# Kernel optimization log

Measured on AMD Instinct MI355X. Metric: run time of the kernel, lower is better.

Reference implementation:

```python
import jax, jax.numpy as jnp
import numpy as np

FT_IN = 40960
VFT_IN = 640


def _sparse_linear(indices, values, W, b, B):
    # y[r] = sum_{k: row[k]==r} values[k] * W[:, col[k]]  + b
    # W: [out, in]; gather columns as rows of W.T -> [nnz, out]
    rows = indices[0]
    cols = indices[1]
    contrib = W.T[cols] * values[:, None]          # [nnz, out]
    acc = jnp.zeros((B, W.shape[0]), dtype=W.dtype).at[rows].add(contrib)
    return acc + b


def setup_inputs() -> dict:
    B = 8192
    NNZ_PER_POS = 32
    NNZ = B * NNZ_PER_POS
    FT_OUT = 256
    key = jax.random.key(0)
    ks = jax.random.split(key, 8)

    def make_indices(k):
        kb, kf = jax.random.split(k)
        bids = jax.random.randint(kb, (NNZ,), 0, B, dtype=jnp.int32)
        fids = jax.random.randint(kf, (NNZ,), 0, FT_IN, dtype=jnp.int32)
        return jnp.stack([bids, fids], axis=0)  # [2, NNZ]

    s = 1.0 / np.sqrt(FT_IN)
    sv = 1.0 / np.sqrt(VFT_IN)
    so = 1.0 / np.sqrt(2 * FT_OUT)
    return {
        "stm_indices": make_indices(ks[0]),
        "nstm_indices": make_indices(ks[1]),
        "values": jnp.ones((NNZ,), dtype=jnp.float32),
        "size": B,
        "ft_w": jax.random.uniform(ks[2], (FT_OUT, FT_IN), jnp.float32, -s, s),
        "ft_b": jax.random.uniform(ks[3], (FT_OUT,), jnp.float32, -s, s),
        "fft_w": jax.random.uniform(ks[4], (FT_OUT, VFT_IN), jnp.float32, -sv, sv),
        "fft_b": jax.random.uniform(ks[5], (FT_OUT,), jnp.float32, -sv, sv),
        "out_w": jax.random.uniform(ks[6], (1, 2 * FT_OUT), jnp.float32, -so, so),
        "out_b": jax.random.uniform(ks[7], (1,), jnp.float32, -so, so),
    }


def reference(stm_indices, nstm_indices, values, size, ft_w, ft_b, fft_w, fft_b, out_w, out_b):
    B = size
    # factorized (virtual) feature indices: column % 640
    v_stm = jnp.stack([stm_indices[0], stm_indices[1] % VFT_IN], axis=0)
    v_nstm = jnp.stack([nstm_indices[0], nstm_indices[1] % VFT_IN], axis=0)

    stm_ft = _sparse_linear(stm_indices, values, ft_w, ft_b, B) + \
             _sparse_linear(v_stm, values, fft_w, fft_b, B) - fft_b  # bias added once in torch? no:
    # NOTE: torch adds both biases (ft.bias and fft.bias); undo the subtraction above.
    stm_ft = stm_ft + fft_b
    nstm_ft = _sparse_linear(nstm_indices, values, ft_w, ft_b, B) + \
              _sparse_linear(v_nstm, values, fft_w, fft_b, B)

    hidden = jnp.clip(jnp.concatenate([stm_ft, nstm_ft], axis=1), 0.0, 1.0)  # [B, 2*ft_out]
    return jax.nn.sigmoid(hidden @ out_w.T + out_b)  # [B, 1]
```

## Files before the change

### kernel.cpp

```cpp
#include <hip/hip_runtime.h>
#include <math.h>

#define FT_OUT 256
#define VFT 640
#define CAP 96

typedef _Float16 half8_t __attribute__((ext_vector_type(8)));
typedef float    float8_t __attribute__((ext_vector_type(8)));

__global__ __launch_bounds__(256) void prep_k(
    const float* __restrict__ ft_w, const float* __restrict__ fft_w,
    _Float16* __restrict__ W2h, int ft_in,
    const int* __restrict__ stm, const int* __restrict__ nstm,
    const float* __restrict__ vals, int nnz,
    int* __restrict__ cnt_s, int* __restrict__ cnt_n,
    int2* __restrict__ slot_s, int2* __restrict__ slot_n, int nfill)
{
    __shared__ float tile[64][65];
    __shared__ float ftile[64][65];
    if ((int)blockIdx.x < nfill) {
        int k = (int)blockIdx.x * 256 + threadIdx.x;
        if (k >= nnz) return;
        int vb = __float_as_int(vals[k]);
        int r = stm[k], c = stm[nnz + k];
        int pos = atomicAdd(&cnt_s[r], 1);
        if (pos < CAP) slot_s[(size_t)r * CAP + pos] = make_int2(c, vb);
        r = nstm[k]; c = nstm[nnz + k];
        pos = atomicAdd(&cnt_n[r], 1);
        if (pos < CAP) slot_n[(size_t)r * CAP + pos] = make_int2(c, vb);
    } else {
        int bx = (int)blockIdx.x - nfill;
        int cb = (bx >> 2) * 64;
        int ob = (bx & 3) * 64;
        int fvb = cb % VFT;
        int tc4 = threadIdx.x & 15, tr = threadIdx.x >> 4;
#pragma unroll
        for (int i = 0; i < 4; i++) {
            int o = i * 16 + tr;
            const float4 f = *(const float4*)(ft_w + (size_t)(ob + o) * ft_in + cb + tc4 * 4);
            const float4 g = *(const float4*)(fft_w + (size_t)(ob + o) * VFT + fvb + tc4 * 4);
            tile[o][tc4 * 4 + 0] = f.x; tile[o][tc4 * 4 + 1] = f.y;
            tile[o][tc4 * 4 + 2] = f.z; tile[o][tc4 * 4 + 3] = f.w;
            ftile[o][tc4 * 4 + 0] = g.x; ftile[o][tc4 * 4 + 1] = g.y;
            ftile[o][tc4 * 4 + 2] = g.z; ftile[o][tc4 * 4 + 3] = g.w;
        }
        __syncthreads();
        int g = threadIdx.x & 7, cl = threadIdx.x >> 3;
#pragma unroll
        for (int i = 0; i < 2; i++) {
            int c = i * 32 + cl, col = cb + c;
            half8_t h;
#pragma unroll
            for (int jj = 0; jj < 8; jj++)
                h[jj] = (_Float16)(tile[g * 8 + jj][c] + ftile[g * 8 + jj][c]);
            *(half8_t*)(W2h + (size_t)col * FT_OUT + ob + g * 8) = h;
        }
    }
}

__global__ __launch_bounds__(256) void fused_k(const _Float16* __restrict__ W2h,
    const int* __restrict__ cnt_s, const int2* __restrict__ slot_s,
    const int* __restrict__ cnt_n, const int2* __restrict__ slot_n,
    const float* __restrict__ ft_b, const float* __restrict__ fft_b,
    const float* __restrict__ out_w, const float* __restrict__ out_b,
    float* __restrict__ out, int B) {
    int lane = threadIdx.x & 63;
    int wid  = threadIdx.x >> 6;
    int row  = blockIdx.x * 2 + (wid >> 1);
    int side = wid & 1;
    int hi   = lane >> 5;
    int sl   = lane & 31;

    const int*  cnt  = side ? cnt_n : cnt_s;
    const int2* slot = (side ? slot_n : slot_s) + (size_t)row * CAP;
    int n = min(cnt[row], CAP);

    float8_t acc;
#pragma unroll
    for (int k = 0; k < 8; k++) acc[k] = 0.f;
    if (hi == 0) {
        const float4* fb = (const float4*)(ft_b + sl * 8);
        const float4* gb = (const float4*)(fft_b + sl * 8);
        float4 a0 = fb[0], a1 = fb[1], c0 = gb[0], c1 = gb[1];
        acc[0] = a0.x + c0.x; acc[1] = a0.y + c0.y; acc[2] = a0.z + c0.z; acc[3] = a0.w + c0.w;
        acc[4] = a1.x + c1.x; acc[5] = a1.y + c1.y; acc[6] = a1.z + c1.z; acc[7] = a1.w + c1.w;
    }

#define PROC(e)                                                                     \
    {                                                                               \
        int   c_ = hi ? (e).z : (e).x;                                              \
        float v_ = __int_as_float(hi ? (e).w : (e).y);                              \
        const half8_t w_ = *(const half8_t*)(W2h + ((size_t)c_ << 8) + (sl << 3));  \
        _Pragma("unroll")                                                           \
        for (int k = 0; k < 8; k++) acc[k] += v_ * (float)w_[k];                    \
    }

    int j = 0;
    for (; j + 8 <= n; j += 8) {
        const int4 e0 = *(const int4*)(slot + j);
        const int4 e1 = *(const int4*)(slot + j + 2);
        const int4 e2 = *(const int4*)(slot + j + 4);
        const int4 e3 = *(const int4*)(slot + j + 6);
        PROC(e0) PROC(e1) PROC(e2) PROC(e3)
    }
    for (; j + 2 <= n; j += 2) {
        const int4 e = *(const int4*)(slot + j);
        PROC(e)
    }
    if (j < n) {
        const int2 e = slot[j];
        int   c_ = hi ? 0 : e.x;
        float v_ = hi ? 0.f : __int_as_float(e.y);
        const half8_t w_ = *(const half8_t*)(W2h + ((size_t)c_ << 8) + (sl << 3));
#pragma unroll
        for (int k = 0; k < 8; k++) acc[k] += v_ * (float)w_[k];
    }
#undef PROC

#pragma unroll
    for (int k = 0; k < 8; k++) {
        float o = __shfl_xor(acc[k], 32, 64);
        acc[k] = fminf(fmaxf(acc[k] + o, 0.f), 1.f);
    }

    const float4* ow = (const float4*)(out_w + side * FT_OUT + sl * 8);
    const float4 w0 = ow[0], w1 = ow[1];
    float p = acc[0] * w0.x + acc[1] * w0.y + acc[2] * w0.z + acc[3] * w0.w
            + acc[4] * w1.x + acc[5] * w1.y + acc[6] * w1.z + acc[7] * w1.w;
#pragma unroll
    for (int m = 32; m >= 1; m >>= 1) p += __shfl_xor(p, m, 64);
    p *= 0.5f;

    __shared__ float part[4];
    if (lane == 0) part[wid] = p;
    __syncthreads();
    if (threadIdx.x < 2) {
        float q = part[threadIdx.x * 2] + part[threadIdx.x * 2 + 1] + out_b[0];
        out[blockIdx.x * 2 + threadIdx.x] = 1.f / (1.f + __expf(-q));
    }
}

extern "C" void kernel_launch(void* const* d_in, const int* in_sizes, int n_in,
                              void* d_out, int out_size, void* d_ws, size_t ws_size,
                              hipStream_t stream) {
    const int*   stm    = (const int*)d_in[0];
    const int*   nstm   = (const int*)d_in[1];
    const float* values = (const float*)d_in[2];
    const float* ft_w   = (const float*)d_in[4];
    const float* ft_b   = (const float*)d_in[5];
    const float* fft_w  = (const float*)d_in[6];
    const float* fft_b  = (const float*)d_in[7];
    const float* out_w  = (const float*)d_in[8];
    const float* out_b  = (const float*)d_in[9];
    float* out = (float*)d_out;

    int B = out_size;
    int nnz = in_sizes[0] / 2;
    int ft_in = in_sizes[4] / FT_OUT;

    _Float16* W2h  = (_Float16*)d_ws;
    int2*  slot_s  = (int2*)(W2h + (size_t)ft_in * FT_OUT);
    int2*  slot_n  = slot_s + (size_t)B * CAP;
    int*   cnt_s   = (int*)(slot_n + (size_t)B * CAP);
    int*   cnt_n   = cnt_s + B;

    int nbuild = (ft_in / 64) * (FT_OUT / 64);
    int nfill  = (nnz + 255) / 256;

    hipMemsetAsync(cnt_s, 0, 2 * (size_t)B * sizeof(int), stream);
    prep_k<<<nfill + nbuild, 256, 0, stream>>>(ft_w, fft_w, W2h, ft_in,
                                               stm, nstm, values, nnz,
                                               cnt_s, cnt_n, slot_s, slot_n, nfill);
    fused_k<<<B / 2, 256, 0, stream>>>(W2h, cnt_s, slot_s, cnt_n, slot_n,
                                       ft_b, fft_b, out_w, out_b, out, B);
}
```

Before: 166.2 us.

## Pack slot entries into 32-bit col/fp16 value and process two nnz per thread

Slot entries shrink from int2 (column, float value) to a single 32-bit word holding the column in the upper 16 bits and the value as fp16 in the lower bits, halving slot traffic in both the fill and the consume kernels. Each fill thread now handles two nonzeros using vectorised loads. The weight transpose pre-adds ft_w and fft_w before writing to a single shared tile, which drops the second shared array. In exchange, columns must fit in 16 bits (40960 does) and values lose precision when rounded to fp16.

```diff
diff --git a/kernel.cpp b/kernel.cpp
--- a/kernel.cpp
+++ b/kernel.cpp
@@ -8,26 +8,39 @@
 typedef _Float16 half8_t __attribute__((ext_vector_type(8)));
 typedef float    float8_t __attribute__((ext_vector_type(8)));
 
+static __device__ __forceinline__ unsigned pack_cv(int c, float v) {
+    _Float16 h = (_Float16)v;
+    unsigned short b = __builtin_bit_cast(unsigned short, h);
+    return ((unsigned)c << 16) | (unsigned)b;
+}
+
 __global__ __launch_bounds__(256) void prep_k(
     const float* __restrict__ ft_w, const float* __restrict__ fft_w,
     _Float16* __restrict__ W2h, int ft_in,
     const int* __restrict__ stm, const int* __restrict__ nstm,
     const float* __restrict__ vals, int nnz,
     int* __restrict__ cnt_s, int* __restrict__ cnt_n,
-    int2* __restrict__ slot_s, int2* __restrict__ slot_n, int nfill)
+    unsigned* __restrict__ slot_s, unsigned* __restrict__ slot_n, int nfill)
 {
     __shared__ float tile[64][65];
-    __shared__ float ftile[64][65];
     if ((int)blockIdx.x < nfill) {
-        int k = (int)blockIdx.x * 256 + threadIdx.x;
+        int k = ((int)blockIdx.x * 256 + (int)threadIdx.x) * 2;
         if (k >= nnz) return;
-        int vb = __float_as_int(vals[k]);
-        int r = stm[k], c = stm[nnz + k];
-        int pos = atomicAdd(&cnt_s[r], 1);
-        if (pos < CAP) slot_s[(size_t)r * CAP + pos] = make_int2(c, vb);
-        r = nstm[k]; c = nstm[nnz + k];
-        pos = atomicAdd(&cnt_n[r], 1);
-        if (pos < CAP) slot_n[(size_t)r * CAP + pos] = make_int2(c, vb);
+        int2   rs = *(const int2*)(stm + k);
+        int2   cs = *(const int2*)(stm + nnz + k);
+        int2   rn = *(const int2*)(nstm + k);
+        int2   cn = *(const int2*)(nstm + nnz + k);
+        float2 v  = *(const float2*)(vals + k);
+        unsigned e0 = pack_cv(cs.x, v.x), e1 = pack_cv(cs.y, v.y);
+        unsigned e2 = pack_cv(cn.x, v.x), e3 = pack_cv(cn.y, v.y);
+        int p0 = atomicAdd(&cnt_s[rs.x], 1);
+        int p1 = atomicAdd(&cnt_s[rs.y], 1);
+        int p2 = atomicAdd(&cnt_n[rn.x], 1);
+        int p3 = atomicAdd(&cnt_n[rn.y], 1);
+        if (p0 < CAP) slot_s[(size_t)rs.x * CAP + p0] = e0;
+        if (p1 < CAP) slot_s[(size_t)rs.y * CAP + p1] = e1;
+        if (p2 < CAP) slot_n[(size_t)rn.x * CAP + p2] = e2;
+        if (p3 < CAP) slot_n[(size_t)rn.y * CAP + p3] = e3;
     } else {
         int bx = (int)blockIdx.x - nfill;
         int cb = (bx >> 2) * 64;
@@ -39,10 +52,8 @@
             int o = i * 16 + tr;
             const float4 f = *(const float4*)(ft_w + (size_t)(ob + o) * ft_in + cb + tc4 * 4);
             const float4 g = *(const float4*)(fft_w + (size_t)(ob + o) * VFT + fvb + tc4 * 4);
-            tile[o][tc4 * 4 + 0] = f.x; tile[o][tc4 * 4 + 1] = f.y;
-            tile[o][tc4 * 4 + 2] = f.z; tile[o][tc4 * 4 + 3] = f.w;
-            ftile[o][tc4 * 4 + 0] = g.x; ftile[o][tc4 * 4 + 1] = g.y;
-            ftile[o][tc4 * 4 + 2] = g.z; ftile[o][tc4 * 4 + 3] = g.w;
+            tile[o][tc4 * 4 + 0] = f.x + g.x; tile[o][tc4 * 4 + 1] = f.y + g.y;
+            tile[o][tc4 * 4 + 2] = f.z + g.z; tile[o][tc4 * 4 + 3] = f.w + g.w;
         }
         __syncthreads();
         int g = threadIdx.x & 7, cl = threadIdx.x >> 3;
@@ -52,15 +63,15 @@
             half8_t h;
 #pragma unroll
             for (int jj = 0; jj < 8; jj++)
-                h[jj] = (_Float16)(tile[g * 8 + jj][c] + ftile[g * 8 + jj][c]);
+                h[jj] = (_Float16)tile[g * 8 + jj][c];
             *(half8_t*)(W2h + (size_t)col * FT_OUT + ob + g * 8) = h;
         }
     }
 }
 
 __global__ __launch_bounds__(256) void fused_k(const _Float16* __restrict__ W2h,
-    const int* __restrict__ cnt_s, const int2* __restrict__ slot_s,
-    const int* __restrict__ cnt_n, const int2* __restrict__ slot_n,
+    const int* __restrict__ cnt_s, const unsigned* __restrict__ slot_s,
+    const int* __restrict__ cnt_n, const unsigned* __restrict__ slot_n,
     const float* __restrict__ ft_b, const float* __restrict__ fft_b,
     const float* __restrict__ out_w, const float* __restrict__ out_b,
     float* __restrict__ out, int B) {
@@ -71,8 +82,8 @@
     int hi   = lane >> 5;
     int sl   = lane & 31;
 
-    const int*  cnt  = side ? cnt_n : cnt_s;
-    const int2* slot = (side ? slot_n : slot_s) + (size_t)row * CAP;
+    const int*      cnt  = side ? cnt_n : cnt_s;
+    const unsigned* slot = (side ? slot_n : slot_s) + (size_t)row * CAP;
     int n = min(cnt[row], CAP);
 
     float8_t acc;
@@ -86,36 +97,47 @@
         acc[4] = a1.x + c1.x; acc[5] = a1.y + c1.y; acc[6] = a1.z + c1.z; acc[7] = a1.w + c1.w;
     }
 
-#define PROC(e)                                                                     \
+#define PROC2(p_, q_)                                                               \
     {                                                                               \
-        int   c_ = hi ? (e).z : (e).x;                                              \
-        float v_ = __int_as_float(hi ? (e).w : (e).y);                              \
+        unsigned u_ = hi ? (q_) : (p_);                                             \
+        int   c_ = (int)(u_ >> 16);                                                 \
+        float v_ = (float)__builtin_bit_cast(_Float16, (unsigned short)(u_ & 0xffffu)); \
         const half8_t w_ = *(const half8_t*)(W2h + ((size_t)c_ << 8) + (sl << 3));  \
         _Pragma("unroll")                                                           \
         for (int k = 0; k < 8; k++) acc[k] += v_ * (float)w_[k];                    \
     }
 
+    const uint4* sp4 = (const uint4*)slot;
     int j = 0;
-    for (; j + 8 <= n; j += 8) {
-        const int4 e0 = *(const int4*)(slot + j);
-        const int4 e1 = *(const int4*)(slot + j + 2);
-        const int4 e2 = *(const int4*)(slot + j + 4);
-        const int4 e3 = *(const int4*)(slot + j + 6);
-        PROC(e0) PROC(e1) PROC(e2) PROC(e3)
+    for (; j + 16 <= n; j += 16) {
+        const uint4 a = sp4[(j >> 2) + 0];
+        const uint4 b = sp4[(j >> 2) + 1];
+        const uint4 c = sp4[(j >> 2) + 2];
+        const uint4 d = sp4[(j >> 2) + 3];
+        PROC2(a.x, a.y) PROC2(a.z, a.w)
+        PROC2(b.x, b.y) PROC2(b.z, b.w)
+        PROC2(c.x, c.y) PROC2(c.z, c.w)
+        PROC2(d.x, d.y) PROC2(d.z, d.w)
     }
-    for (; j + 2 <= n; j += 2) {
-        const int4 e = *(const int4*)(slot + j);
-        PROC(e)
+    for (; j + 4 <= n; j += 4) {
+        const uint4 a = sp4[j >> 2];
+        PROC2(a.x, a.y) PROC2(a.z, a.w)
+    }
+    if (j + 2 <= n) {
+        const uint2 a = *(const uint2*)(slot + j);
+        PROC2(a.x, a.y)
+        j += 2;
     }
     if (j < n) {
-        const int2 e = slot[j];
-        int   c_ = hi ? 0 : e.x;
-        float v_ = hi ? 0.f : __int_as_float(e.y);
+        unsigned u = slot[j];
+        int   c_ = hi ? 0 : (int)(u >> 16);
+        float v_ = hi ? 0.f
+                      : (float)__builtin_bit_cast(_Float16, (unsigned short)(u & 0xffffu));
         const half8_t w_ = *(const half8_t*)(W2h + ((size_t)c_ << 8) + (sl << 3));
 #pragma unroll
         for (int k = 0; k < 8; k++) acc[k] += v_ * (float)w_[k];
     }
-#undef PROC
+#undef PROC2
 
 #pragma unroll
     for (int k = 0; k < 8; k++) {
@@ -158,14 +180,14 @@
     int nnz = in_sizes[0] / 2;
     int ft_in = in_sizes[4] / FT_OUT;
 
-    _Float16* W2h  = (_Float16*)d_ws;
-    int2*  slot_s  = (int2*)(W2h + (size_t)ft_in * FT_OUT);
-    int2*  slot_n  = slot_s + (size_t)B * CAP;
-    int*   cnt_s   = (int*)(slot_n + (size_t)B * CAP);
-    int*   cnt_n   = cnt_s + B;
+    _Float16* W2h    = (_Float16*)d_ws;
+    unsigned* slot_s = (unsigned*)(W2h + (size_t)ft_in * FT_OUT);
+    unsigned* slot_n = slot_s + (size_t)B * CAP;
+    int*      cnt_s  = (int*)(slot_n + (size_t)B * CAP);
+    int*      cnt_n  = cnt_s + B;
 
     int nbuild = (ft_in / 64) * (FT_OUT / 64);
-    int nfill  = (nnz + 255) / 256;
+    int nfill  = (nnz / 2 + 255) / 256;
 
     hipMemsetAsync(cnt_s, 0, 2 * (size_t)B * sizeof(int), stream);
     prep_k<<<nfill + nbuild, 256, 0, stream>>>(ft_w, fft_w, W2h, ft_in,
```

Result: no change. 165.0 us (-0.7%).
